# Optimization experiments

Measured on AMD Instinct MI355X. Metric: run time of the kernel, lower is better.

The kernel has to match this reference:

```python
import jax, jax.numpy as jnp
import numpy as np

NMS_THRESH = 0.7
N_PRE = 12000
N_POST = 2000
IMG_X, IMG_Y = 1333.0, 402.0
MIN_SIZE = 16.0
FEAT_X, FEAT_Y, N_ANCH = 83, 25, 9   # int(1333/16), int(402/16), 9 anchors/cell
A = FEAT_X * FEAT_Y * N_ANCH         # 18675 anchors
CHUNK = 600                          # N_PRE % CHUNK == 0 -> 20 scan steps


def _make_anchors():
    stride = 16.0
    scales = np.array([8.0, 16.0, 32.0])
    ratios = np.array([0.5, 1.0, 2.0])
    hs = (stride * scales[:, None] * np.sqrt(ratios)[None, :]).ravel()  # 9 heights
    ws = (stride * scales[:, None] / np.sqrt(ratios)[None, :]).ravel()  # 9 widths
    cx = (np.arange(FEAT_X, dtype=np.float64) + 0.5) * stride
    cy = (np.arange(FEAT_Y, dtype=np.float64) + 0.5) * stride
    cxg, cyg = np.meshgrid(cx, cy, indexing="ij")  # [83,25]
    cxg = cxg[:, :, None]
    cyg = cyg[:, :, None]
    boxes = np.stack([cxg - 0.5 * ws, cyg - 0.5 * hs,
                      cxg + 0.5 * ws, cyg + 0.5 * hs], axis=-1)  # [83,25,9,4]
    return boxes.reshape(-1, 4).astype(np.float32)


def setup_inputs() -> dict:
    key = jax.random.key(0)
    k1, k2 = jax.random.split(key)
    return {
        "anchor_boxes": jnp.asarray(_make_anchors()),                          # [A,4]
        "rpn_cls_score": jax.random.normal(k1, (1, A, 2), jnp.float32),        # [B,A,2]
        "rpn_bbox_pred": jax.random.normal(k2, (1, A, 4), jnp.float32) * 0.1,  # [B,A,4]
    }


def _decode(anchor_boxes, rpn_cls_score, rpn_bbox_pred):
    # anchor geometry (same conventions as original: y from col1/3, x from col0/2)
    h_a = anchor_boxes[:, 3] - anchor_boxes[:, 1]
    w_a = anchor_boxes[:, 2] - anchor_boxes[:, 0]
    cy_a = anchor_boxes[:, 1] + 0.5 * h_a
    cx_a = anchor_boxes[:, 0] + 0.5 * w_a
    dx = rpn_bbox_pred[..., 0]
    dy = rpn_bbox_pred[..., 1]
    dw = rpn_bbox_pred[..., 2]
    dh = rpn_bbox_pred[..., 3]
    cy = dy * h_a + cy_a
    cx = dx * w_a + cx_a
    h = jnp.exp(dh) * h_a
    w = jnp.exp(dw) * w_a
    # clip: x coords to image_size[0], y coords to image_size[1] (as in original)
    x1 = jnp.clip(cx - 0.5 * w, 0.0, IMG_X)
    x2 = jnp.clip(cx + 0.5 * w, 0.0, IMG_X)
    y1 = jnp.clip(cy - 0.5 * h, 0.0, IMG_Y)
    y2 = jnp.clip(cy + 0.5 * h, 0.0, IMG_Y)
    roi = jnp.stack([x1, y1, x2, y2], axis=-1)  # [B,A,4]
    valid = ((y2 - y1) >= MIN_SIZE) & ((x2 - x1) >= MIN_SIZE)  # [B,A]
    score = rpn_cls_score[..., 1]  # objectness = channel 1 of 2-class score
    return roi, score, valid


def _nms_per_image(roi, score, valid):
    # sort valid boxes by descending score, take top N_PRE
    score = jnp.where(valid, score, -jnp.inf)
    order = jnp.argsort(-score)[:N_PRE]
    boxes = roi[order]  # [N_PRE,4]
    x1, y1, x2, y2 = boxes[:, 0], boxes[:, 1], boxes[:, 2], boxes[:, 3]
    areas = (x2 - x1 + 1.0) * (y2 - y1 + 1.0)
    idx = jnp.arange(N_PRE)

    def chunk_step(mark, zs):
        def row(z):
            xx1 = jnp.maximum(x1[z], x1)
            yy1 = jnp.maximum(y1[z], y1)
            xx2 = jnp.minimum(x2[z], x2)
            yy2 = jnp.minimum(y2[z], y2)
            w = jnp.maximum(0.0, xx2 - xx1 + 1.0)
            h = jnp.maximum(0.0, yy2 - yy1 + 1.0)
            inter = w * h
            ovr = inter / (areas[z] + areas - inter)
            over = ovr >= NMS_THRESH
            # faithful to original: np.where on the slice [z+1:] yields indices
            # RELATIVE to the slice, which are then used as absolute row indices.
            # So box k is deleted iff exists z with IoU(box z, box z+1+k) >= thresh.
            src = idx + z + 1
            contrib = jnp.where(src < N_PRE, over[jnp.minimum(src, N_PRE - 1)], False)
            return contrib & (z < N_PRE - 1)  # loop runs z in range(N_PRE-1)
        contribs = jax.vmap(row)(zs)  # [CHUNK, N_PRE]
        return mark | contribs.any(axis=0), None

    mark0 = jnp.zeros((N_PRE,), bool)
    mark, _ = jax.lax.scan(chunk_step, mark0, idx.reshape(-1, CHUNK))
    keep = ~mark
    # compact kept boxes to the front (stable), truncate to N_POST
    ord2 = jnp.argsort((~keep).astype(jnp.int32), stable=True)[:N_POST]
    kept = keep[ord2]
    out = jnp.where(kept[:, None], boxes[ord2], 0.0)  # zero-pad deleted slots
    return out, kept


def reference(anchor_boxes, rpn_cls_score, rpn_bbox_pred):
    roi, score, valid = _decode(anchor_boxes, rpn_cls_score, rpn_bbox_pred)
    rois, kept = jax.vmap(_nms_per_image)(roi, score, valid)
    return rois, kept  # [B,N_POST,4], [B,N_POST]
```

## Files before the change

### kernel.cpp

```cpp
#include <hip/hip_runtime.h>
#include <math.h>

#define A_TOT   18675
#define N_PRE   12000
#define N_POST  2000
#define IMG_X   1333.0f
#define IMG_Y   402.0f
#define MIN_SZ  16.0f
#define NMS_T   0.7f

#define IPT     4
#define JT      256
#define JCHUNK  512

__global__ void decode_kernel(const float* __restrict__ anch,
                              const float* __restrict__ cls,
                              const float* __restrict__ pred,
                              float4* __restrict__ roi,
                              unsigned long long* __restrict__ key,
                              int* __restrict__ rank) {
    int i = blockIdx.x * blockDim.x + threadIdx.x;
    if (i >= A_TOT) return;

    float ax1 = anch[4*i+0], ay1 = anch[4*i+1], ax2 = anch[4*i+2], ay2 = anch[4*i+3];
    float h_a  = __fsub_rn(ay2, ay1);
    float w_a  = __fsub_rn(ax2, ax1);
    float cy_a = __fadd_rn(ay1, __fmul_rn(0.5f, h_a));
    float cx_a = __fadd_rn(ax1, __fmul_rn(0.5f, w_a));

    float dx = pred[4*i+0], dy = pred[4*i+1], dw = pred[4*i+2], dh = pred[4*i+3];

    float cy = __fadd_rn(__fmul_rn(dy, h_a), cy_a);
    float cx = __fadd_rn(__fmul_rn(dx, w_a), cx_a);
    float h  = __fmul_rn(expf(dh), h_a);
    float w  = __fmul_rn(expf(dw), w_a);

    float hw = __fmul_rn(0.5f, w);
    float hh = __fmul_rn(0.5f, h);
    float x1 = fminf(fmaxf(__fsub_rn(cx, hw), 0.0f), IMG_X);
    float x2 = fminf(fmaxf(__fadd_rn(cx, hw), 0.0f), IMG_X);
    float y1 = fminf(fmaxf(__fsub_rn(cy, hh), 0.0f), IMG_Y);
    float y2 = fminf(fmaxf(__fadd_rn(cy, hh), 0.0f), IMG_Y);

    bool valid = (__fsub_rn(y2, y1) >= MIN_SZ) && (__fsub_rn(x2, x1) >= MIN_SZ);

    roi[i] = make_float4(x1, y1, x2, y2);

    float s = valid ? cls[2*i+1] : -INFINITY;
    unsigned ub   = __float_as_uint(s);
    unsigned mask = ((unsigned)((int)ub >> 31)) | 0x80000000u;
    unsigned ord  = ub ^ mask;
    unsigned kd   = ~ord;
    key[i]  = ((unsigned long long)kd << 32) | (unsigned)i;
    rank[i] = 0;
}

__global__ void rank2_kernel(const unsigned long long* __restrict__ key,
                             int* __restrict__ rank) {
    __shared__ unsigned long long kls[JT];
    const int t    = threadIdx.x;
    const int ib   = blockIdx.x * (256 * IPT);
    const int jbeg = blockIdx.y * JCHUNK;
    const int jend = min(A_TOT, jbeg + JCHUNK);

    unsigned long long ki[IPT];
    int idx[IPT];
#pragma unroll
    for (int e = 0; e < IPT; ++e) {
        int i  = ib + e * 256 + t;
        idx[e] = i;
        ki[e]  = (i < A_TOT) ? key[i] : 0ull;
    }
    int cnt[IPT] = {0, 0, 0, 0};

    for (int jb = jbeg; jb < jend; jb += JT) {
        int j = jb + t;
        kls[t] = (j < jend) ? key[j] : ~0ull;
        __syncthreads();
#pragma unroll 32
        for (int tt = 0; tt < JT; ++tt) {
            unsigned long long kj = kls[tt];
#pragma unroll
            for (int e = 0; e < IPT; ++e)
                cnt[e] += (kj < ki[e]) ? 1 : 0;
        }
        __syncthreads();
    }
#pragma unroll
    for (int e = 0; e < IPT; ++e)
        if (idx[e] < A_TOT && cnt[e]) atomicAdd(&rank[idx[e]], cnt[e]);
}

__global__ void scatter_kernel(const int* __restrict__ rank,
                               const float4* __restrict__ roi,
                               float4* __restrict__ sboxes,
                               float* __restrict__ sareas) {
    int i = blockIdx.x * blockDim.x + threadIdx.x;
    if (i >= A_TOT) return;
    int r = rank[i];
    if (r < N_PRE) {
        float4 b = roi[i];
        sboxes[r] = b;
        sareas[r] = __fmul_rn(__fadd_rn(__fsub_rn(b.z, b.x), 1.0f),
                              __fadd_rn(__fsub_rn(b.w, b.y), 1.0f));
    }
}

__global__ void nms_kernel(const float4* __restrict__ sboxes,
                           const float* __restrict__ sareas,
                           unsigned* __restrict__ mark) {
    int wid  = (blockIdx.x * blockDim.x + threadIdx.x) >> 6;
    int lane = threadIdx.x & 63;
    if (wid >= N_PRE) return;
    const int i      = wid;
    const int npairs = N_PRE - 1 - i;

    bool found = false;
    for (int base = 0; base < npairs; base += 64) {
        int z = base + lane;
        bool over = false;
        if (z < npairs) {
            float4 bz = sboxes[z];
            float4 bj = sboxes[z + i + 1];
            float az = sareas[z];
            float aj = sareas[z + i + 1];
            float xx1 = fmaxf(bz.x, bj.x);
            float yy1 = fmaxf(bz.y, bj.y);
            float xx2 = fminf(bz.z, bj.z);
            float yy2 = fminf(bz.w, bj.w);
            float w = fmaxf(0.0f, __fadd_rn(__fsub_rn(xx2, xx1), 1.0f));
            float h = fmaxf(0.0f, __fadd_rn(__fsub_rn(yy2, yy1), 1.0f));
            float inter = __fmul_rn(w, h);
            float denom = __fsub_rn(__fadd_rn(az, aj), inter);
            float ovr   = __fdiv_rn(inter, denom);
            over = (ovr >= NMS_T);
        }
        if (__any(over)) { found = true; break; }
    }
    if (lane == 0) mark[i] = found ? 1u : 0u;
}

__global__ void output_kernel(const unsigned* __restrict__ mark,
                              const float4* __restrict__ sboxes,
                              float* __restrict__ out) {
    __shared__ int lds[1024];
    __shared__ int s_total;
    const int t = threadIdx.x;
    const int E = 12;
    const int i0 = t * E;

    bool keep[E];
    int cnt = 0;
#pragma unroll
    for (int e = 0; e < E; ++e) {
        int i = i0 + e;
        bool k = (i < N_PRE) && (mark[i] == 0u);
        keep[e] = k;
        cnt += k ? 1 : 0;
    }
    lds[t] = cnt;
    __syncthreads();
    for (int off = 1; off < 1024; off <<= 1) {
        int x = (t >= off) ? lds[t - off] : 0;
        __syncthreads();
        lds[t] += x;
        __syncthreads();
    }
    int incl = lds[t];
    int base = incl - cnt;
    if (t == 1023) s_total = incl;
    __syncthreads();
    const int total = s_total;

    int pos = base;
#pragma unroll
    for (int e = 0; e < E; ++e) {
        if (keep[e] && pos < N_POST) {
            float4 b = sboxes[i0 + e];
            out[4*pos+0] = b.x;
            out[4*pos+1] = b.y;
            out[4*pos+2] = b.z;
            out[4*pos+3] = b.w;
            out[4*N_POST + pos] = 1.0f;
        }
        pos += keep[e] ? 1 : 0;
    }
    for (int p = t; p < N_POST; p += 1024) {
        if (p >= total) {
            out[4*p+0] = 0.0f; out[4*p+1] = 0.0f;
            out[4*p+2] = 0.0f; out[4*p+3] = 0.0f;
            out[4*N_POST + p] = 0.0f;
        }
    }
}

extern "C" void kernel_launch(void* const* d_in, const int* in_sizes, int n_in,
                              void* d_out, int out_size, void* d_ws, size_t ws_size,
                              hipStream_t stream) {
    const float* anch = (const float*)d_in[0];
    const float* cls  = (const float*)d_in[1];
    const float* pred = (const float*)d_in[2];
    float* out = (float*)d_out;

    char* ws = (char*)d_ws;
    float4*             roi    = (float4*)(ws + 0);
    int*                rank   = (int*)   (ws + 298800);
    unsigned long long* key    = (unsigned long long*)(ws + 373504);
    float4*             sboxes = (float4*)(ws + 373504);
    float*              sareas = (float*) (ws + 565504);
    unsigned*           mark   = (unsigned*)(ws + 613504);

    const int TB = 256;
    const int ablk = (A_TOT + TB - 1) / TB;
    const int nIblk = (A_TOT + 256*IPT - 1) / (256*IPT);
    const int njc   = (A_TOT + JCHUNK - 1) / JCHUNK;

    decode_kernel<<<ablk, TB, 0, stream>>>(anch, cls, pred, roi, key, rank);
    rank2_kernel<<<dim3(nIblk, njc), TB, 0, stream>>>(key, rank);
    scatter_kernel<<<ablk, TB, 0, stream>>>(rank, roi, sboxes, sareas);
    nms_kernel<<<(N_PRE * 64) / TB, TB, 0, stream>>>(sboxes, sareas, mark);
    output_kernel<<<1, 1024, 0, stream>>>(mark, sboxes, out);
}
```

Baseline: 56.09 us.

## Replace all-pairs rank sort with 16-bit bucket histogram and intra-bucket ranking

Replaces the O(N^2) all-pairs key comparison used to rank scores with a radix-style approach: a 65536-bucket histogram built in decode, a single-block prefix scan, an atomic bucket scatter, then per-element ranking only within its own bucket. This removes the quadratic comparison kernel. In exchange it adds a memset, a serial single-block scan over 64K buckets, and atomics. Per-element work becomes data-dependent and degrades if many keys share a bucket.

```diff
diff --git a/kernel.cpp b/kernel.cpp
--- a/kernel.cpp
+++ b/kernel.cpp
@@ -8,17 +8,14 @@
 #define IMG_Y   402.0f
 #define MIN_SZ  16.0f
 #define NMS_T   0.7f
-
-#define IPT     4
-#define JT      256
-#define JCHUNK  512
+#define NBUCK   65536
 
 __global__ void decode_kernel(const float* __restrict__ anch,
                               const float* __restrict__ cls,
                               const float* __restrict__ pred,
                               float4* __restrict__ roi,
                               unsigned long long* __restrict__ key,
-                              int* __restrict__ rank) {
+                              unsigned* __restrict__ hist) {
     int i = blockIdx.x * blockDim.x + threadIdx.x;
     if (i >= A_TOT) return;
 
@@ -51,58 +48,73 @@
     unsigned mask = ((unsigned)((int)ub >> 31)) | 0x80000000u;
     unsigned ord  = ub ^ mask;
     unsigned kd   = ~ord;
-    key[i]  = ((unsigned long long)kd << 32) | (unsigned)i;
-    rank[i] = 0;
-}
-
-__global__ void rank2_kernel(const unsigned long long* __restrict__ key,
-                             int* __restrict__ rank) {
-    __shared__ unsigned long long kls[JT];
-    const int t    = threadIdx.x;
-    const int ib   = blockIdx.x * (256 * IPT);
-    const int jbeg = blockIdx.y * JCHUNK;
-    const int jend = min(A_TOT, jbeg + JCHUNK);
-
-    unsigned long long ki[IPT];
-    int idx[IPT];
-#pragma unroll
-    for (int e = 0; e < IPT; ++e) {
-        int i  = ib + e * 256 + t;
-        idx[e] = i;
-        ki[e]  = (i < A_TOT) ? key[i] : 0ull;
-    }
-    int cnt[IPT] = {0, 0, 0, 0};
-
-    for (int jb = jbeg; jb < jend; jb += JT) {
-        int j = jb + t;
-        kls[t] = (j < jend) ? key[j] : ~0ull;
-        __syncthreads();
-#pragma unroll 32
-        for (int tt = 0; tt < JT; ++tt) {
-            unsigned long long kj = kls[tt];
-#pragma unroll
-            for (int e = 0; e < IPT; ++e)
-                cnt[e] += (kj < ki[e]) ? 1 : 0;
-        }
-        __syncthreads();
-    }
-#pragma unroll
-    for (int e = 0; e < IPT; ++e)
-        if (idx[e] < A_TOT && cnt[e]) atomicAdd(&rank[idx[e]], cnt[e]);
-}
-
-__global__ void scatter_kernel(const int* __restrict__ rank,
-                               const float4* __restrict__ roi,
-                               float4* __restrict__ sboxes,
-                               float* __restrict__ sareas) {
+    key[i] = ((unsigned long long)kd << 32) | (unsigned)i;
+    atomicAdd(&hist[kd >> 16], 1u);
+}
+
+__global__ void scan_kernel(const unsigned* __restrict__ hist,
+                            unsigned* __restrict__ bstart,
+                            unsigned* __restrict__ bcur) {
+    __shared__ unsigned part[1024];
+    const int t = threadIdx.x;
+    const int base = t * 64;
+
+    unsigned v[64];
+    unsigned s = 0;
+#pragma unroll
+    for (int e = 0; e < 64; ++e) { v[e] = hist[base + e]; s += v[e]; }
+    part[t] = s;
+    __syncthreads();
+    for (int off = 1; off < 1024; off <<= 1) {
+        unsigned x = (t >= off) ? part[t - off] : 0u;
+        __syncthreads();
+        part[t] += x;
+        __syncthreads();
+    }
+    unsigned run = (t == 0) ? 0u : part[t - 1];
+#pragma unroll
+    for (int e = 0; e < 64; ++e) {
+        bstart[base + e] = run;
+        bcur[base + e]   = run;
+        run += v[e];
+    }
+}
+
+__global__ void bucket_scatter_kernel(const unsigned long long* __restrict__ key,
+                                      unsigned* __restrict__ bcur,
+                                      unsigned long long* __restrict__ bkey) {
     int i = blockIdx.x * blockDim.x + threadIdx.x;
     if (i >= A_TOT) return;
-    int r = rank[i];
+    unsigned long long Ki = key[i];
+    unsigned b = (unsigned)(Ki >> 48);
+    unsigned pos = atomicAdd(&bcur[b], 1u);
+    bkey[pos] = Ki;
+}
+
+__global__ void rankscatter_kernel(const unsigned long long* __restrict__ key,
+                                   const unsigned* __restrict__ hist,
+                                   const unsigned* __restrict__ bstart,
+                                   const unsigned long long* __restrict__ bkey,
+                                   const float4* __restrict__ roi,
+                                   float4* __restrict__ sboxes,
+                                   float* __restrict__ sareas) {
+    int i = blockIdx.x * blockDim.x + threadIdx.x;
+    if (i >= A_TOT) return;
+    unsigned long long Ki = key[i];
+    unsigned b = (unsigned)(Ki >> 48);
+    unsigned start = bstart[b];
+    if (start >= N_PRE) return;
+    unsigned cnt = hist[b];
+    unsigned r = start;
+    if (cnt > 1) {
+        for (unsigned m = 0; m < cnt; ++m)
+            r += (bkey[start + m] < Ki) ? 1u : 0u;
+    }
     if (r < N_PRE) {
-        float4 b = roi[i];
-        sboxes[r] = b;
-        sareas[r] = __fmul_rn(__fadd_rn(__fsub_rn(b.z, b.x), 1.0f),
-                              __fadd_rn(__fsub_rn(b.w, b.y), 1.0f));
+        float4 bx = roi[i];
+        sboxes[r] = bx;
+        sareas[r] = __fmul_rn(__fadd_rn(__fsub_rn(bx.z, bx.x), 1.0f),
+                              __fadd_rn(__fsub_rn(bx.w, bx.y), 1.0f));
     }
 }
 
@@ -204,20 +216,23 @@
 
     char* ws = (char*)d_ws;
     float4*             roi    = (float4*)(ws + 0);
-    int*                rank   = (int*)   (ws + 298800);
-    unsigned long long* key    = (unsigned long long*)(ws + 373504);
-    float4*             sboxes = (float4*)(ws + 373504);
-    float*              sareas = (float*) (ws + 565504);
-    unsigned*           mark   = (unsigned*)(ws + 613504);
+    unsigned long long* key    = (unsigned long long*)(ws + 299008);
+    unsigned*           hist   = (unsigned*)(ws + 448512);
+    unsigned*           bstart = (unsigned*)(ws + 710656);
+    unsigned*           bcur   = (unsigned*)(ws + 972800);
+    unsigned long long* bkey   = (unsigned long long*)(ws + 1234944);
+    float4*             sboxes = (float4*)(ws + 1384448);
+    float*              sareas = (float*)(ws + 1576448);
+    unsigned*           mark   = (unsigned*)(ws + 1624448);
 
     const int TB = 256;
     const int ablk = (A_TOT + TB - 1) / TB;
-    const int nIblk = (A_TOT + 256*IPT - 1) / (256*IPT);
-    const int njc   = (A_TOT + JCHUNK - 1) / JCHUNK;
-
-    decode_kernel<<<ablk, TB, 0, stream>>>(anch, cls, pred, roi, key, rank);
-    rank2_kernel<<<dim3(nIblk, njc), TB, 0, stream>>>(key, rank);
-    scatter_kernel<<<ablk, TB, 0, stream>>>(rank, roi, sboxes, sareas);
+
+    hipMemsetAsync(hist, 0, NBUCK * sizeof(unsigned), stream);
+    decode_kernel<<<ablk, TB, 0, stream>>>(anch, cls, pred, roi, key, hist);
+    scan_kernel<<<1, 1024, 0, stream>>>(hist, bstart, bcur);
+    bucket_scatter_kernel<<<ablk, TB, 0, stream>>>(key, bcur, bkey);
+    rankscatter_kernel<<<ablk, TB, 0, stream>>>(key, hist, bstart, bkey, roi, sboxes, sareas);
     nms_kernel<<<(N_PRE * 64) / TB, TB, 0, stream>>>(sboxes, sareas, mark);
     output_kernel<<<1, 1024, 0, stream>>>(mark, sboxes, out);
 }
```

Result: slower. 78.75 us (+40.4%).
